# Optimization experiments

Measured on AMD Instinct MI355X. Metric: run time of the kernel, lower is better.

## Reference

```python
import jax, jax.numpy as jnp
import numpy as np

NL, D, NH, HD, MLP, L = 4, 1280, 16, 80, 5120, 2048
SEG = 512  # patches per packed image


def setup_inputs() -> dict:
    key = jax.random.key(0)
    ks = jax.random.split(key, 16)
    s = 0.02
    # per-segment RoPE frequency table: positions restart at each image boundary
    inv_freq = 1.0 / (10000.0 ** (jnp.arange(0, HD, 2, dtype=jnp.float32) / HD))  # (HD/2,)
    pos = (jnp.arange(L) % SEG).astype(jnp.float32)
    rotary_pos_emb = pos[:, None] * inv_freq[None, :]  # (L, HD/2)
    return {
        "x": jax.random.normal(ks[0], (L, D), jnp.float32),
        "rotary_pos_emb": rotary_pos_emb,
        "cu_seqlens": jnp.array([0, 512, 1024, 1536, 2048], jnp.int32),
        "ln1_g": 1.0 + s * jax.random.normal(ks[1], (NL, D), jnp.float32),
        "ln1_b": s * jax.random.normal(ks[2], (NL, D), jnp.float32),
        "ln2_g": 1.0 + s * jax.random.normal(ks[3], (NL, D), jnp.float32),
        "ln2_b": s * jax.random.normal(ks[4], (NL, D), jnp.float32),
        "qkv_w": s * jax.random.normal(ks[5], (NL, 3 * D, D), jnp.float32),
        "qkv_b": s * jax.random.normal(ks[6], (NL, 3 * D), jnp.float32),
        "proj_w": s * jax.random.normal(ks[7], (NL, D, D), jnp.float32),
        "proj_b": s * jax.random.normal(ks[8], (NL, D), jnp.float32),
        "mlp_w1": s * jax.random.normal(ks[9], (NL, MLP, D), jnp.float32),
        "mlp_b1": s * jax.random.normal(ks[10], (NL, MLP), jnp.float32),
        "mlp_w2": s * jax.random.normal(ks[11], (NL, D, MLP), jnp.float32),
        "mlp_b2": s * jax.random.normal(ks[12], (NL, D), jnp.float32),
    }


def _ln(x, g, b):
    m = jnp.mean(x, axis=-1, keepdims=True)
    v = jnp.mean((x - m) ** 2, axis=-1, keepdims=True)
    return (x - m) * jax.lax.rsqrt(v + 1e-6) * g + b


def _rope(t, cos, sin):
    # t: (L, H, HD); cos/sin: (L, 1, HD)
    half = t.shape[-1] // 2
    rot = jnp.concatenate([-t[..., half:], t[..., :half]], axis=-1)
    return t * cos + rot * sin


def reference(x, rotary_pos_emb, cu_seqlens, ln1_g, ln1_b, ln2_g, ln2_b,
              qkv_w, qkv_b, proj_w, proj_b, mlp_w1, mlp_b1, mlp_w2, mlp_b2):
    Lx = x.shape[0]
    cos = jnp.cos(rotary_pos_emb)
    sin = jnp.sin(rotary_pos_emb)
    cos = jnp.concatenate([cos, cos], axis=-1)[:, None, :]  # (L,1,HD)
    sin = jnp.concatenate([sin, sin], axis=-1)[:, None, :]
    # block-diagonal attention mask from cu_seqlens via segment ids
    seg = jnp.searchsorted(cu_seqlens, jnp.arange(Lx), side="right")  # (L,)
    mask = seg[:, None] == seg[None, :]  # (L,L) bool
    neg = jnp.finfo(jnp.float32).min
    scale = 1.0 / np.sqrt(HD)
    for l in range(qkv_w.shape[0]):
        h = _ln(x, ln1_g[l], ln1_b[l])
        qkv = (h @ qkv_w[l].T + qkv_b[l]).reshape(Lx, 3, NH, HD)
        q, k, v = qkv[:, 0], qkv[:, 1], qkv[:, 2]  # (L,H,HD) each
        q = _rope(q, cos, sin)
        k = _rope(k, cos, sin)
        scores = jnp.einsum("lhd,mhd->hlm", q, k) * scale  # (H,L,L)
        scores = jnp.where(mask[None], scores, neg)
        w = jax.nn.softmax(scores.astype(jnp.float32), axis=-1).astype(x.dtype)
        att = jnp.einsum("hlm,mhd->lhd", w, v).reshape(Lx, NH * HD)
        x = x + att @ proj_w[l].T + proj_b[l]
        h = _ln(x, ln2_g[l], ln2_b[l])
        x = x + jax.nn.gelu(h @ mlp_w1[l].T + mlp_b1[l], approximate=True) @ mlp_w2[l].T + mlp_b2[l]
    return x
```

## Files before the change

kernel.cpp:

```cpp
#include <hip/hip_runtime.h>
#include <cstdint>
#include <cstddef>

typedef unsigned short u16;
typedef __bf16 bf16_t;
typedef bf16_t bf16x8 __attribute__((ext_vector_type(8)));
typedef float f32x4 __attribute__((ext_vector_type(4)));

#define NLAY 4
#define DMODEL 1280
#define NHEAD 16
#define HDIM 80
#define HDP 96
#define MLPD 5120
#define LTOK 2048
#define SEGLEN 512

__device__ __forceinline__ u16 f2bf(float f) {
  union { float f; unsigned u; } x; x.f = f;
  unsigned r = x.u + 0x7fffu + ((x.u >> 16) & 1u);
  return (u16)(r >> 16);
}
__device__ __forceinline__ float bf2f(u16 s) {
  union { unsigned u; float f; } x; x.u = ((unsigned)s) << 16;
  return x.f;
}

#define GLOAD_LDS16(gsrc, ldst) \
  __builtin_amdgcn_global_load_lds((const __attribute__((address_space(1))) void*)(gsrc), \
                                   (__attribute__((address_space(3))) void*)(ldst), 16, 0, 0)

__device__ __forceinline__ void barrier_mem() {
  asm volatile("s_barrier" ::: "memory");
}

#define C0 (3 * DMODEL * DMODEL / 4)
#define C1 (C0 + DMODEL * DMODEL / 4)
#define C2 (C1 + MLPD * DMODEL / 4)
#define C3 (C2 + DMODEL * MLPD / 4)
__global__ __launch_bounds__(256) void cvt4(const float* __restrict__ s_q,
                                            const float* __restrict__ s_p,
                                            const float* __restrict__ s_1,
                                            const float* __restrict__ s_2,
                                            u16* __restrict__ o_q, u16* __restrict__ o_p,
                                            u16* __restrict__ o_1, u16* __restrict__ o_2) {
  int i = blockIdx.x * 256 + threadIdx.x;
  const float* src; u16* dst; int off;
  if (i < C0)      { src = s_q; dst = o_q; off = i; }
  else if (i < C1) { src = s_p; dst = o_p; off = i - C0; }
  else if (i < C2) { src = s_1; dst = o_1; off = i - C1; }
  else if (i < C3) { src = s_2; dst = o_2; off = i - C2; }
  else return;
  const float4 v = reinterpret_cast<const float4*>(src)[off];
  union { u16 s[4]; uint2 u; } o;
  o.s[0] = f2bf(v.x); o.s[1] = f2bf(v.y); o.s[2] = f2bf(v.z); o.s[3] = f2bf(v.w);
  reinterpret_cast<uint2*>(dst)[off] = o.u;
}

__global__ __launch_bounds__(256) void ln_bf16(const float* __restrict__ x,
                                               const float* __restrict__ g,
                                               const float* __restrict__ b,
                                               u16* __restrict__ out) {
  int row = blockIdx.x;
  int t = threadIdx.x;
  const float* xr = x + (size_t)row * DMODEL;
  float v[5]; float s = 0.f, s2 = 0.f;
#pragma unroll
  for (int i = 0; i < 5; i++) { v[i] = xr[t + i * 256]; s += v[i]; s2 += v[i] * v[i]; }
#pragma unroll
  for (int off = 32; off; off >>= 1) { s += __shfl_down(s, off); s2 += __shfl_down(s2, off); }
  __shared__ float ps[4], ps2[4];
  int w = t >> 6;
  if ((t & 63) == 0) { ps[w] = s; ps2[w] = s2; }
  __syncthreads();
  s = ps[0] + ps[1] + ps[2] + ps[3];
  s2 = ps2[0] + ps2[1] + ps2[2] + ps2[3];
  float mean = s * (1.f / DMODEL);
  float var = s2 * (1.f / DMODEL) - mean * mean;
  float inv = rsqrtf(var + 1e-6f);
#pragma unroll
  for (int i = 0; i < 5; i++) {
    int c = t + i * 256;
    out[(size_t)row * DMODEL + c] = f2bf((v[i] - mean) * inv * g[c] + b[c]);
  }
}

template <int EPI>
__global__ __launch_bounds__(512) void gemm8(const u16* __restrict__ A,
                                             const u16* __restrict__ B,
                                             const float* __restrict__ bias,
                                             u16* __restrict__ Cb,
                                             int M, int N, int K) {
  __shared__ u16 As[3][256 * 64];
  __shared__ u16 Bs[3][128 * 64];

  int gN = gridDim.x, gM = gridDim.y;
  int flat = blockIdx.x + gN * blockIdx.y;
  int nwg = gN * gM;
  int qc = nwg >> 3, rc = nwg & 7;
  int xcd = flat & 7, pos = flat >> 3;
  int start = (xcd < rc) ? xcd * (qc + 1) : rc * (qc + 1) + (xcd - rc) * qc;
  int swz = start + pos;
  int m0 = (swz % gM) * 256;
  int n0 = (swz / gM) * 128;

  int t = threadIdx.x, lane = t & 63, w = t >> 6;
  int wm = w >> 1, wn = w & 1;
  int r = lane & 15, kq = lane >> 4;
  f32x4 acc[4][4] = {};

  auto stageA = [&](int buf, int k0, int half) {
#pragma unroll
    for (int i = 0; i < 2; i++) {
      int chunk = half * 1024 + i * 512 + t;
      int row = chunk >> 3, s = chunk & 7;
      int ss = s ^ (row & 7);
      GLOAD_LDS16(A + (size_t)(m0 + row) * K + k0 + ss * 8, &As[buf][chunk * 8]);
    }
  };
  auto stageB = [&](int buf, int k0) {
#pragma unroll
    for (int i = 0; i < 2; i++) {
      int chunk = i * 512 + t;
      int row = chunk >> 3, s = chunk & 7;
      int ss = s ^ (row & 7);
      GLOAD_LDS16(B + (size_t)(n0 + row) * K + k0 + ss * 8, &Bs[buf][chunk * 8]);
    }
  };

  bf16x8 af[2][2], bf[2][2];
  auto loadA = [&](const u16* as, int mh) {
#pragma unroll
    for (int i2 = 0; i2 < 2; i2++)
#pragma unroll
      for (int ks = 0; ks < 2; ks++) {
        int row = wm * 64 + (2 * mh + i2) * 16 + r;
        int sx8 = (ks * 4 + kq) ^ (r & 7);
        af[i2][ks] = *(const bf16x8*)&as[row * 64 + sx8 * 8];
      }
  };
  auto loadB = [&](const u16* bs, int nh) {
#pragma unroll
    for (int j2 = 0; j2 < 2; j2++)
#pragma unroll
      for (int ks = 0; ks < 2; ks++) {
        int row = wn * 64 + (2 * nh + j2) * 16 + r;
        int sx8 = (ks * 4 + kq) ^ (r & 7);
        bf[j2][ks] = *(const bf16x8*)&bs[row * 64 + sx8 * 8];
      }
  };
  auto mfma8 = [&](int mh, int nh) {
    __builtin_amdgcn_s_setprio(1);
#pragma unroll
    for (int i2 = 0; i2 < 2; i2++)
#pragma unroll
      for (int j2 = 0; j2 < 2; j2++)
#pragma unroll
        for (int ks = 0; ks < 2; ks++)
          acc[2 * mh + i2][2 * nh + j2] = __builtin_amdgcn_mfma_f32_16x16x32_bf16(
              af[i2][ks], bf[j2][ks], acc[2 * mh + i2][2 * nh + j2], 0, 0, 0);
    __builtin_amdgcn_s_setprio(0);
  };

  int NT = K >> 6;
  stageA(0, 0, 0); stageA(0, 0, 1); stageB(0, 0);
  stageA(1, 64, 0); stageA(1, 64, 1); stageB(1, 64);

  int bt = 0;
  for (int kt = 0; kt < NT; kt++) {
    if (kt == NT - 1) asm volatile("s_waitcnt vmcnt(0)" ::: "memory");
    else              asm volatile("s_waitcnt vmcnt(6)" ::: "memory");
    barrier_mem();
    const u16* as = As[bt];
    const u16* bs = Bs[bt];
    int b2 = bt + 2; if (b2 >= 3) b2 -= 3;
    int k2 = (kt + 2) << 6;
    bool st = (kt + 2) < NT;
    loadA(as, 0); loadB(bs, 0);
    if (st) stageA(b2, k2, 0);
    mfma8(0, 0);
    barrier_mem();
    loadB(bs, 1);
    if (st) stageA(b2, k2, 1);
    mfma8(0, 1);
    barrier_mem();
    loadA(as, 1);
    if (st) stageB(b2, k2);
    mfma8(1, 1);
    barrier_mem();
    loadB(bs, 0);
    mfma8(1, 0);
    bt++; if (bt == 3) bt = 0;
  }

#pragma unroll
  for (int i = 0; i < 4; i++) {
#pragma unroll
    for (int j = 0; j < 4; j++) {
      int col = n0 + wn * 64 + j * 16 + r;
      float bv = bias[col];
#pragma unroll
      for (int reg = 0; reg < 4; reg++) {
        int rowg = m0 + wm * 64 + i * 16 + kq * 4 + reg;
        float val = acc[i][j][reg] + bv;
        if (EPI == 2) {
          float z2 = -1.5957691216057308f * fmaf(0.044715f * val, val * val, val);
          float gg = val / (1.f + __expf(z2));
          Cb[(size_t)rowg * N + col] = f2bf(gg);
        } else {
          Cb[(size_t)rowg * N + col] = f2bf(val);
        }
      }
    }
  }
}

template <int EPI, int BM, int BN>
__global__ __launch_bounds__(256) void gemm_bt(const u16* __restrict__ A,
                                               const u16* __restrict__ B,
                                               const float* __restrict__ bias,
                                               float* __restrict__ Cf,
                                               u16* __restrict__ Cb,
                                               int M, int N, int K) {
  constexpr int MI = BM / 32;
  constexpr int NJ = BN / 32;
  constexpr int ACH = BM * 64 / (256 * 8);
  constexpr int BCH = BN * 64 / (256 * 8);
  __shared__ u16 As[2][BM * 64];
  __shared__ u16 Bs[2][BN * 64];

  int gN = gridDim.x, gM = gridDim.y;
  int flat = blockIdx.x + gN * blockIdx.y;
  int nwg = gN * gM;
  int qc = nwg >> 3, rc = nwg & 7;
  int xcd = flat & 7, pos = flat >> 3;
  int start = (xcd < rc) ? xcd * (qc + 1) : rc * (qc + 1) + (xcd - rc) * qc;
  int swz = start + pos;
  int m0 = (swz % gM) * BM;
  int n0 = (swz / gM) * BN;

  int t = threadIdx.x, lane = t & 63, w = t >> 6;
  int wm = w >> 1, wn = w & 1;
  int r = lane & 15, kq = lane >> 4;
  f32x4 acc[MI][NJ] = {};

  auto stage = [&](int buf, int k0) {
#pragma unroll
    for (int i = 0; i < ACH; i++) {
      int chunk = i * 256 + t;
      int row = chunk >> 3, s = chunk & 7;
      int ss = s ^ (row & 7);
      GLOAD_LDS16(A + (size_t)(m0 + row) * K + k0 + ss * 8, &As[buf][chunk * 8]);
    }
#pragma unroll
    for (int i = 0; i < BCH; i++) {
      int chunk = i * 256 + t;
      int row = chunk >> 3, s = chunk & 7;
      int ss = s ^ (row & 7);
      GLOAD_LDS16(B + (size_t)(n0 + row) * K + k0 + ss * 8, &Bs[buf][chunk * 8]);
    }
  };

  auto compute = [&](int buf) {
#pragma unroll
    for (int kk = 0; kk < 64; kk += 32) {
      int sx8 = (((kk >> 3) + kq) ^ (r & 7)) * 8;
      bf16x8 af[MI], bfr[NJ];
#pragma unroll
      for (int i = 0; i < MI; i++)
        af[i] = *(const bf16x8*)&As[buf][(wm * (BM / 2) + i * 16 + r) * 64 + sx8];
#pragma unroll
      for (int j = 0; j < NJ; j++)
        bfr[j] = *(const bf16x8*)&Bs[buf][(wn * (BN / 2) + j * 16 + r) * 64 + sx8];
#pragma unroll
      for (int i = 0; i < MI; i++)
#pragma unroll
        for (int j = 0; j < NJ; j++)
          acc[i][j] = __builtin_amdgcn_mfma_f32_16x16x32_bf16(af[i], bfr[j], acc[i][j], 0, 0, 0);
    }
  };

  int NT = K >> 6;
  stage(0, 0);
  __syncthreads();
  for (int step = 0; step < NT; step++) {
    int buf = step & 1;
    if (step + 1 < NT) stage(buf ^ 1, (step + 1) * 64);
    compute(buf);
    __syncthreads();
  }

#pragma unroll
  for (int i = 0; i < MI; i++) {
#pragma unroll
    for (int j = 0; j < NJ; j++) {
      int col = n0 + wn * (BN / 2) + j * 16 + r;
      float bv = bias[col];
#pragma unroll
      for (int reg = 0; reg < 4; reg++) {
        int rowg = m0 + wm * (BM / 2) + i * 16 + kq * 4 + reg;
        float val = acc[i][j][reg] + bv;
        if (EPI == 1) {
          Cf[(size_t)rowg * N + col] += val;
        } else {
          Cb[(size_t)rowg * N + col] = f2bf(val);
        }
      }
    }
  }
}

__global__ __launch_bounds__(256) void rope_pack(const u16* __restrict__ qkv,
                                                 const float* __restrict__ rpe,
                                                 u16* __restrict__ qp,
                                                 u16* __restrict__ kp) {
  int l = blockIdx.x;
  int t = threadIdx.x;
  __shared__ float cs[40], sn[40];
  if (t < 40) {
    float a = rpe[l * 40 + t];
    cs[t] = cosf(a);
    sn[t] = sinf(a);
  }
  __syncthreads();
  const u16* row = qkv + (size_t)l * (3 * DMODEL);
  const float scale = 0.11180339887498949f;
#pragma unroll
  for (int i = 0; i < 5; i++) {
    int e = t + i * 256;
    int h = e / HDIM, d = e - h * HDIM;
    int dm = (d < 40) ? d : d - 40;
    float c = cs[dm], s = sn[dm];
    float qv = bf2f(row[h * HDIM + d]);
    float qr = (d < 40) ? -bf2f(row[h * HDIM + d + 40]) : bf2f(row[h * HDIM + d - 40]);
    qp[((size_t)h * LTOK + l) * HDP + d] = f2bf((qv * c + qr * s) * scale);
    float kv = bf2f(row[DMODEL + h * HDIM + d]);
    float kr = (d < 40) ? -bf2f(row[DMODEL + h * HDIM + d + 40]) : bf2f(row[DMODEL + h * HDIM + d - 40]);
    kp[((size_t)h * LTOK + l) * HDP + d] = f2bf(kv * c + kr * s);
  }
  {
    int h = t >> 4, p = t & 15;
    qp[((size_t)h * LTOK + l) * HDP + HDIM + p] = 0;
    kp[((size_t)h * LTOK + l) * HDP + HDIM + p] = 0;
  }
}

__global__ __launch_bounds__(256) void vtrans(const u16* __restrict__ qkv,
                                              u16* __restrict__ vt) {
  int blk = blockIdx.x;
  int h = blk >> 5, lt = blk & 31;
  int t = threadIdx.x;
  __shared__ u16 ld[64][81];
#pragma unroll
  for (int i = 0; i < 20; i++) {
    int idx = t + i * 256;
    int ll = idx / HDIM, d = idx - ll * HDIM;
    ld[ll][d] = qkv[(size_t)(lt * 64 + ll) * (3 * DMODEL) + 2 * DMODEL + h * HDIM + d];
  }
  __syncthreads();
#pragma unroll
  for (int i = 0; i < 20; i++) {
    int idx = t + i * 256;
    int d = idx >> 6, ll = idx & 63;
    vt[((size_t)h * HDIM + d) * LTOK + lt * 64 + ll] = ld[ll][d];
  }
}

__global__ __launch_bounds__(256) void attn(const u16* __restrict__ qp,
                                            const u16* __restrict__ kp,
                                            const u16* __restrict__ vt,
                                            u16* __restrict__ out) {
  int bid = blockIdx.x;
  int h = bid >> 5;
  int seg = (bid >> 3) & 3;
  int qt = bid & 7;
  int t = threadIdx.x, w = t >> 6, lane = t & 63;
  int r = lane & 15, kq = lane >> 4;
  __shared__ u16 P[4][16][512];
  int seg0 = seg * SEGLEN;
  int q0 = seg0 + qt * 64 + w * 16;

  bf16x8 qf[3];
  const u16* qrow = qp + ((size_t)h * LTOK + q0 + r) * HDP;
#pragma unroll
  for (int kk = 0; kk < 3; kk++) qf[kk] = *(const bf16x8*)(qrow + kk * 32 + kq * 8);

  f32x4 sc[32];
#pragma unroll
  for (int j = 0; j < 32; j++) {
    f32x4 a = {0.f, 0.f, 0.f, 0.f};
    const u16* krow = kp + ((size_t)h * LTOK + seg0 + j * 16 + r) * HDP;
#pragma unroll
    for (int kk = 0; kk < 3; kk++) {
      bf16x8 bfr = *(const bf16x8*)(krow + kk * 32 + kq * 8);
      a = __builtin_amdgcn_mfma_f32_16x16x32_bf16(qf[kk], bfr, a, 0, 0, 0);
    }
    sc[j] = a;
  }

#pragma unroll
  for (int rr = 0; rr < 4; rr++) {
    float m = -1e30f;
#pragma unroll
    for (int j = 0; j < 32; j++) m = fmaxf(m, sc[j][rr]);
#pragma unroll
    for (int off = 1; off < 16; off <<= 1) m = fmaxf(m, __shfl_xor(m, off));
    float s = 0.f;
#pragma unroll
    for (int j = 0; j < 32; j++) { float e = __expf(sc[j][rr] - m); sc[j][rr] = e; s += e; }
#pragma unroll
    for (int off = 1; off < 16; off <<= 1) s += __shfl_xor(s, off);
    float inv = 1.f / s;
#pragma unroll
    for (int j = 0; j < 32; j++)
      P[w][kq * 4 + rr][j * 16 + r] = f2bf(sc[j][rr] * inv);
  }
  __syncthreads();

  f32x4 oc[5] = {};
#pragma unroll
  for (int tt = 0; tt < 16; tt++) {
    bf16x8 a = *(const bf16x8*)&P[w][r][tt * 32 + kq * 8];
#pragma unroll
    for (int n = 0; n < 5; n++) {
      const u16* vrow = vt + ((size_t)h * HDIM + n * 16 + r) * LTOK + seg0 + tt * 32 + kq * 8;
      bf16x8 bfr = *(const bf16x8*)vrow;
      oc[n] = __builtin_amdgcn_mfma_f32_16x16x32_bf16(a, bfr, oc[n], 0, 0, 0);
    }
  }
#pragma unroll
  for (int n = 0; n < 5; n++)
#pragma unroll
    for (int reg = 0; reg < 4; reg++) {
      int l = q0 + kq * 4 + reg;
      out[(size_t)l * DMODEL + h * HDIM + n * 16 + r] = f2bf(oc[n][reg]);
    }
}

extern "C" void kernel_launch(void* const* d_in, const int* in_sizes, int n_in,
                              void* d_out, int out_size, void* d_ws, size_t ws_size,
                              hipStream_t stream) {
  (void)in_sizes; (void)n_in; (void)out_size; (void)ws_size;
  const float* x_in   = (const float*)d_in[0];
  const float* rpe    = (const float*)d_in[1];
  const float* ln1_g  = (const float*)d_in[3];
  const float* ln1_b  = (const float*)d_in[4];
  const float* ln2_g  = (const float*)d_in[5];
  const float* ln2_b  = (const float*)d_in[6];
  const float* qkv_w  = (const float*)d_in[7];
  const float* qkv_b  = (const float*)d_in[8];
  const float* proj_w = (const float*)d_in[9];
  const float* proj_b = (const float*)d_in[10];
  const float* mlp_w1 = (const float*)d_in[11];
  const float* mlp_b1 = (const float*)d_in[12];
  const float* mlp_w2 = (const float*)d_in[13];
  const float* mlp_b2 = (const float*)d_in[14];
  float* x = (float*)d_out;

  char* ws = (char*)d_ws;
  size_t off = 0;
  auto alloc = [&](size_t bytes) -> char* {
    char* p = ws + off;
    off = (off + bytes + 255) & ~(size_t)255;
    return p;
  };
  u16* wq  = (u16*)alloc((size_t)3 * DMODEL * DMODEL * 2);
  u16* wp  = (u16*)alloc((size_t)DMODEL * DMODEL * 2);
  u16* w1  = (u16*)alloc((size_t)MLPD * DMODEL * 2);
  u16* w2  = (u16*)alloc((size_t)DMODEL * MLPD * 2);
  u16* hb  = (u16*)alloc((size_t)LTOK * DMODEL * 2);
  u16* qkvb = (u16*)alloc((size_t)LTOK * 3 * DMODEL * 2);
  u16* qp  = (u16*)alloc((size_t)NHEAD * LTOK * HDP * 2);
  u16* kp  = (u16*)alloc((size_t)NHEAD * LTOK * HDP * 2);
  u16* vt  = (u16*)alloc((size_t)NHEAD * HDIM * LTOK * 2);
  u16* att = (u16*)alloc((size_t)LTOK * DMODEL * 2);
  u16* ge  = (u16*)alloc((size_t)LTOK * MLPD * 2);

  hipMemcpyAsync(x, x_in, (size_t)LTOK * DMODEL * sizeof(float),
                 hipMemcpyDeviceToDevice, stream);

  for (int l = 0; l < NLAY; l++) {
    cvt4<<<(C3 + 255) / 256, 256, 0, stream>>>(
        qkv_w + (size_t)l * 3 * DMODEL * DMODEL, proj_w + (size_t)l * DMODEL * DMODEL,
        mlp_w1 + (size_t)l * MLPD * DMODEL, mlp_w2 + (size_t)l * DMODEL * MLPD,
        wq, wp, w1, w2);

    ln_bf16<<<LTOK, 256, 0, stream>>>(x, ln1_g + l * DMODEL, ln1_b + l * DMODEL, hb);
    gemm8<3><<<dim3(30, 8), 512, 0, stream>>>(
        hb, wq, qkv_b + (size_t)l * 3 * DMODEL, qkvb, LTOK, 3 * DMODEL, DMODEL);
    rope_pack<<<LTOK, 256, 0, stream>>>(qkvb, rpe, qp, kp);
    vtrans<<<NHEAD * 32, 256, 0, stream>>>(qkvb, vt);
    attn<<<NHEAD * 4 * 8, 256, 0, stream>>>(qp, kp, vt, att);
    gemm_bt<1, 64, 64><<<dim3(20, 32), 256, 0, stream>>>(
        att, wp, proj_b + (size_t)l * DMODEL, x, nullptr, LTOK, DMODEL, DMODEL);
    ln_bf16<<<LTOK, 256, 0, stream>>>(x, ln2_g + l * DMODEL, ln2_b + l * DMODEL, hb);
    gemm8<2><<<dim3(40, 8), 512, 0, stream>>>(
        hb, w1, mlp_b1 + (size_t)l * MLPD, ge, LTOK, MLPD, DMODEL);
    gemm_bt<1, 64, 64><<<dim3(20, 32), 256, 0, stream>>>(
        ge, w2, mlp_b2 + (size_t)l * DMODEL, x, nullptr, LTOK, DMODEL, MLPD);
  }
}
```

Baseline: 1.019 ms.

## Switch QKV and MLP-up GEMMs to 256x256 tiles with 32-wide K steps

Replaces the 256x128 tile GEMM (K-step 64) with a 256x256 tile kernel using K-step 32. Each wave now computes a 128x64 output with 32 accumulators, and the loop has two MFMA phases per K-step instead of four. The aim is higher arithmetic intensity per tile and fewer barriers per FLOP. The cost is half as many workgroups (120 and 160 blocks on a 256-CU part, so under one wave of work), more accumulator registers, and twice as many K iterations.

After: 1.003 ms. No clear change (-1.6%).

```diff
diff --git a/kernel.cpp b/kernel.cpp
--- a/kernel.cpp
+++ b/kernel.cpp
@@ -86,13 +86,13 @@
 }
 
 template <int EPI>
-__global__ __launch_bounds__(512) void gemm8(const u16* __restrict__ A,
-                                             const u16* __restrict__ B,
-                                             const float* __restrict__ bias,
-                                             u16* __restrict__ Cb,
-                                             int M, int N, int K) {
-  __shared__ u16 As[3][256 * 64];
-  __shared__ u16 Bs[3][128 * 64];
+__global__ __launch_bounds__(512, 2) void gemm256(const u16* __restrict__ A,
+                                                  const u16* __restrict__ B,
+                                                  const float* __restrict__ bias,
+                                                  u16* __restrict__ Cb,
+                                                  int M, int N, int K) {
+  __shared__ u16 As[3][256 * 32];
+  __shared__ u16 Bs[3][256 * 32];
 
   int gN = gridDim.x, gM = gridDim.y;
   int flat = blockIdx.x + gN * blockIdx.y;
@@ -102,19 +102,19 @@
   int start = (xcd < rc) ? xcd * (qc + 1) : rc * (qc + 1) + (xcd - rc) * qc;
   int swz = start + pos;
   int m0 = (swz % gM) * 256;
-  int n0 = (swz / gM) * 128;
+  int n0 = (swz / gM) * 256;
 
   int t = threadIdx.x, lane = t & 63, w = t >> 6;
-  int wm = w >> 1, wn = w & 1;
+  int wm = w >> 2, wn = w & 3;
   int r = lane & 15, kq = lane >> 4;
-  f32x4 acc[4][4] = {};
-
-  auto stageA = [&](int buf, int k0, int half) {
+  f32x4 acc[8][4] = {};
+
+  auto stageA = [&](int buf, int k0) {
 #pragma unroll
     for (int i = 0; i < 2; i++) {
-      int chunk = half * 1024 + i * 512 + t;
-      int row = chunk >> 3, s = chunk & 7;
-      int ss = s ^ (row & 7);
+      int chunk = i * 512 + t;
+      int row = chunk >> 2, s = chunk & 3;
+      int ss = s ^ ((row >> 1) & 3);
       GLOAD_LDS16(A + (size_t)(m0 + row) * K + k0 + ss * 8, &As[buf][chunk * 8]);
     }
   };
@@ -122,86 +122,77 @@
 #pragma unroll
     for (int i = 0; i < 2; i++) {
       int chunk = i * 512 + t;
-      int row = chunk >> 3, s = chunk & 7;
-      int ss = s ^ (row & 7);
+      int row = chunk >> 2, s = chunk & 3;
+      int ss = s ^ ((row >> 1) & 3);
       GLOAD_LDS16(B + (size_t)(n0 + row) * K + k0 + ss * 8, &Bs[buf][chunk * 8]);
     }
   };
 
-  bf16x8 af[2][2], bf[2][2];
-  auto loadA = [&](const u16* as, int mh) {
-#pragma unroll
-    for (int i2 = 0; i2 < 2; i2++)
-#pragma unroll
-      for (int ks = 0; ks < 2; ks++) {
-        int row = wm * 64 + (2 * mh + i2) * 16 + r;
-        int sx8 = (ks * 4 + kq) ^ (r & 7);
-        af[i2][ks] = *(const bf16x8*)&as[row * 64 + sx8 * 8];
-      }
-  };
-  auto loadB = [&](const u16* bs, int nh) {
-#pragma unroll
-    for (int j2 = 0; j2 < 2; j2++)
-#pragma unroll
-      for (int ks = 0; ks < 2; ks++) {
-        int row = wn * 64 + (2 * nh + j2) * 16 + r;
-        int sx8 = (ks * 4 + kq) ^ (r & 7);
-        bf[j2][ks] = *(const bf16x8*)&bs[row * 64 + sx8 * 8];
-      }
-  };
-  auto mfma8 = [&](int mh, int nh) {
-    __builtin_amdgcn_s_setprio(1);
-#pragma unroll
-    for (int i2 = 0; i2 < 2; i2++)
-#pragma unroll
-      for (int j2 = 0; j2 < 2; j2++)
-#pragma unroll
-        for (int ks = 0; ks < 2; ks++)
-          acc[2 * mh + i2][2 * nh + j2] = __builtin_amdgcn_mfma_f32_16x16x32_bf16(
-              af[i2][ks], bf[j2][ks], acc[2 * mh + i2][2 * nh + j2], 0, 0, 0);
-    __builtin_amdgcn_s_setprio(0);
-  };
-
-  int NT = K >> 6;
-  stageA(0, 0, 0); stageA(0, 0, 1); stageB(0, 0);
-  stageA(1, 64, 0); stageA(1, 64, 1); stageB(1, 64);
+  int NT = K >> 5;
+  stageA(0, 0); stageB(0, 0);
+  stageA(1, 32); stageB(1, 32);
 
   int bt = 0;
   for (int kt = 0; kt < NT; kt++) {
-    if (kt == NT - 1) asm volatile("s_waitcnt vmcnt(0)" ::: "memory");
-    else              asm volatile("s_waitcnt vmcnt(6)" ::: "memory");
+    if (kt >= NT - 2) asm volatile("s_waitcnt vmcnt(0)" ::: "memory");
+    else              asm volatile("s_waitcnt vmcnt(4)" ::: "memory");
     barrier_mem();
     const u16* as = As[bt];
     const u16* bs = Bs[bt];
     int b2 = bt + 2; if (b2 >= 3) b2 -= 3;
-    int k2 = (kt + 2) << 6;
     bool st = (kt + 2) < NT;
-    loadA(as, 0); loadB(bs, 0);
-    if (st) stageA(b2, k2, 0);
-    mfma8(0, 0);
+    int k2 = (kt + 2) << 5;
+
+    bf16x8 af[8], bfr[2];
+#pragma unroll
+    for (int i = 0; i < 8; i++) {
+      int row = wm * 128 + i * 16 + r;
+      int ss = kq ^ ((row >> 1) & 3);
+      af[i] = *(const bf16x8*)&as[row * 32 + ss * 8];
+    }
+#pragma unroll
+    for (int j = 0; j < 2; j++) {
+      int row = wn * 64 + j * 16 + r;
+      int ss = kq ^ ((row >> 1) & 3);
+      bfr[j] = *(const bf16x8*)&bs[row * 32 + ss * 8];
+    }
+    if (st) stageA(b2, k2);
+    __builtin_amdgcn_s_setprio(1);
+#pragma unroll
+    for (int i = 0; i < 8; i++)
+#pragma unroll
+      for (int j = 0; j < 2; j++)
+        acc[i][j] = __builtin_amdgcn_mfma_f32_16x16x32_bf16(af[i], bfr[j], acc[i][j], 0, 0, 0);
+    __builtin_amdgcn_s_setprio(0);
     barrier_mem();
-    loadB(bs, 1);
-    if (st) stageA(b2, k2, 1);
-    mfma8(0, 1);
-    barrier_mem();
-    loadA(as, 1);
+
+#pragma unroll
+    for (int j = 0; j < 2; j++) {
+      int row = wn * 64 + (j + 2) * 16 + r;
+      int ss = kq ^ ((row >> 1) & 3);
+      bfr[j] = *(const bf16x8*)&bs[row * 32 + ss * 8];
+    }
     if (st) stageB(b2, k2);
-    mfma8(1, 1);
-    barrier_mem();
-    loadB(bs, 0);
-    mfma8(1, 0);
+    __builtin_amdgcn_s_setprio(1);
+#pragma unroll
+    for (int i = 0; i < 8; i++)
+#pragma unroll
+      for (int j = 0; j < 2; j++)
+        acc[i][j + 2] = __builtin_amdgcn_mfma_f32_16x16x32_bf16(af[i], bfr[j], acc[i][j + 2], 0, 0, 0);
+    __builtin_amdgcn_s_setprio(0);
+
     bt++; if (bt == 3) bt = 0;
   }
 
 #pragma unroll
-  for (int i = 0; i < 4; i++) {
+  for (int i = 0; i < 8; i++) {
 #pragma unroll
     for (int j = 0; j < 4; j++) {
       int col = n0 + wn * 64 + j * 16 + r;
       float bv = bias[col];
 #pragma unroll
       for (int reg = 0; reg < 4; reg++) {
-        int rowg = m0 + wm * 64 + i * 16 + kq * 4 + reg;
+        int rowg = m0 + wm * 128 + i * 16 + kq * 4 + reg;
         float val = acc[i][j][reg] + bv;
         if (EPI == 2) {
           float z2 = -1.5957691216057308f * fmaf(0.044715f * val, val * val, val);
@@ -486,7 +477,7 @@
         wq, wp, w1, w2);
 
     ln_bf16<<<LTOK, 256, 0, stream>>>(x, ln1_g + l * DMODEL, ln1_b + l * DMODEL, hb);
-    gemm8<3><<<dim3(30, 8), 512, 0, stream>>>(
+    gemm256<3><<<dim3(15, 8), 512, 0, stream>>>(
         hb, wq, qkv_b + (size_t)l * 3 * DMODEL, qkvb, LTOK, 3 * DMODEL, DMODEL);
     rope_pack<<<LTOK, 256, 0, stream>>>(qkvb, rpe, qp, kp);
     vtrans<<<NHEAD * 32, 256, 0, stream>>>(qkvb, vt);
@@ -494,7 +485,7 @@
     gemm_bt<1, 64, 64><<<dim3(20, 32), 256, 0, stream>>>(
         att, wp, proj_b + (size_t)l * DMODEL, x, nullptr, LTOK, DMODEL, DMODEL);
     ln_bf16<<<LTOK, 256, 0, stream>>>(x, ln2_g + l * DMODEL, ln2_b + l * DMODEL, hb);
-    gemm8<2><<<dim3(40, 8), 512, 0, stream>>>(
+    gemm256<2><<<dim3(20, 8), 512, 0, stream>>>(
         hb, w1, mlp_b1 + (size_t)l * MLPD, ge, LTOK, MLPD, DMODEL);
     gemm_bt<1, 64, 64><<<dim3(20, 32), 256, 0, stream>>>(
         ge, w2, mlp_b2 + (size_t)l * DMODEL, x, nullptr, LTOK, DMODEL, MLPD);
```
